# Optimization experiments

Measured on AMD Instinct MI355X. Metric: run time of the kernel, lower is better.

## Reference

```python
import jax, jax.numpy as jnp
import numpy as np

B, N, D, H, L = 2, 2048, 128, 8, 3
V = 32          # NUM_ATOM_TYPES (assumed)
DH = D // H
SCALE = 1.0 / (DH ** 0.5)
NEG = -1e9      # stands in for -inf in the additive attention mask
EPS = 1e-5


def _ln(x, g, b):
    m = x.mean(-1, keepdims=True)
    v = ((x - m) ** 2).mean(-1, keepdims=True)
    return (x - m) / jnp.sqrt(v + EPS) * g + b


def setup_inputs() -> dict:
    key = jax.random.key(0)
    ks = jax.random.split(key, 24)
    nrm = lambda k, shape, std=0.02: jax.random.normal(k, shape, jnp.float32) * std
    atom_embed = nrm(ks[0], (V, D)).at[0].set(0.0)  # padding_idx = 0
    cons_embed = nrm(ks[1], (1, 1, D))
    in_w = nrm(ks[2], (D, D)); in_b = jnp.zeros((D,), jnp.float32)
    qkv_w = nrm(ks[3], (L, 3 * D, D)); qkv_b = jnp.zeros((L, 3 * D), jnp.float32)
    out_w = nrm(ks[4], (L, D, D)); out_b = jnp.zeros((L, D), jnp.float32)
    ln1_g = jnp.ones((L, D), jnp.float32); ln1_b = jnp.zeros((L, D), jnp.float32)
    ln2_g = jnp.ones((L, D), jnp.float32); ln2_b = jnp.zeros((L, D), jnp.float32)
    ff1_w = nrm(ks[5], (L, 4 * D, D)); ff1_b = jnp.zeros((L, 4 * D), jnp.float32)
    ff2_w = nrm(ks[6], (L, D, 4 * D)); ff2_b = jnp.zeros((L, D), jnp.float32)
    struct_bias = nrm(ks[7], (L,), 0.5)  # scalar per layer (init 0 in torch; randomized to exercise the path)
    head_ln_g = jnp.ones((D,), jnp.float32); head_ln_b = jnp.zeros((D,), jnp.float32)
    head_w = nrm(ks[8], (1, D)); head_b = jnp.zeros((1,), jnp.float32)
    is_atom = jax.random.bernoulli(ks[9], 0.5, (B, N))
    atom_id = jax.random.randint(ks[10], (B, N), 0, V)
    mask = jax.random.bernoulli(ks[11], 0.9, (B, N))
    adjacency = (jax.random.uniform(ks[12], (B, N, N)) < 0.002).astype(jnp.float32)
    adjacency = jnp.maximum(adjacency, jnp.eye(N, dtype=jnp.float32)[None])  # self-loops
    root_idx = jax.random.randint(ks[13], (B,), 0, N)
    return dict(atom_embed=atom_embed, cons_embed=cons_embed, in_w=in_w, in_b=in_b,
                qkv_w=qkv_w, qkv_b=qkv_b, out_w=out_w, out_b=out_b,
                ln1_g=ln1_g, ln1_b=ln1_b, ln2_g=ln2_g, ln2_b=ln2_b,
                ff1_w=ff1_w, ff1_b=ff1_b, ff2_w=ff2_w, ff2_b=ff2_b,
                struct_bias=struct_bias, head_ln_g=head_ln_g, head_ln_b=head_ln_b,
                head_w=head_w, head_b=head_b, adjacency=adjacency,
                is_atom=is_atom, atom_id=atom_id, mask=mask, root_idx=root_idx)


def reference(atom_embed, cons_embed, in_w, in_b, qkv_w, qkv_b, out_w, out_b,
              ln1_g, ln1_b, ln2_g, ln2_b, ff1_w, ff1_b, ff2_w, ff2_b,
              struct_bias, head_ln_g, head_ln_b, head_w, head_b,
              adjacency, is_atom, atom_id, mask, root_idx):
    # node embeddings
    ae = atom_embed[jnp.clip(atom_id, 0, V - 1)]                     # [B,N,D]
    h = jnp.where(is_atom[..., None], ae, jnp.broadcast_to(cons_embed, (B, N, D)))
    h = h @ in_w.T + in_b
    # additive attention mask: valid pairs OK; invalid query rows attend only to self
    pair_ok = mask[:, :, None] & mask[:, None, :]
    eye = jnp.eye(N, dtype=bool)[None]
    ok = pair_ok | ((~mask)[:, :, None] & eye)
    am = jnp.where(ok, 0.0, NEG).astype(jnp.float32)                 # [B,N,N]
    for i in range(L):
        x = _ln(h, ln1_g[i], ln1_b[i])
        qkv = (x @ qkv_w[i].T + qkv_b[i]).reshape(B, N, 3, H, DH)
        q, k, v = (jnp.transpose(qkv[:, :, j], (0, 2, 1, 3)) for j in range(3))  # [B,H,N,DH]
        scores = jnp.einsum('bhqd,bhkd->bhqk', q, k) * SCALE \
                 + struct_bias[i] * adjacency[:, None] + am[:, None]
        attn = jax.nn.softmax(scores, axis=-1)
        o = jnp.einsum('bhqk,bhkd->bhqd', attn, v)
        o = jnp.transpose(o, (0, 2, 1, 3)).reshape(B, N, D)
        h = h + (o @ out_w[i].T + out_b[i])
        x2 = _ln(h, ln2_g[i], ln2_b[i])
        f = jax.nn.gelu(x2 @ ff1_w[i].T + ff1_b[i], approximate=False)
        h = h + (f @ ff2_w[i].T + ff2_b[i])
    pooled = h[jnp.arange(B), root_idx]                              # [B,D]
    p = _ln(pooled, head_ln_g, head_ln_b)
    return (p @ head_w.T + head_b)[:, 0]                             # [B]
```

## Files before the change

### kernel.cpp

```cpp
#include <hip/hip_runtime.h>
#include <cmath>

#define NB 2
#define NN 2048
#define ND 128
#define NH 8
#define NL 3
#define NV 32
#define NDH 16
#define LN_EPS 1e-5f
#define QSCALE 0.36067376022224085f

typedef __bf16 bf8_t __attribute__((ext_vector_type(8)));
typedef __bf16 bf4_t __attribute__((ext_vector_type(4)));
typedef float f4x __attribute__((ext_vector_type(4)));
typedef float f16x __attribute__((ext_vector_type(16)));

struct CastArgs {
  const float* s[5];
  __bf16* d[5];
  int startblk[5];
};
__global__ __launch_bounds__(256) void prep_kernel(
    CastArgs a, const float* __restrict__ adj, unsigned long long* __restrict__ abits,
    const int* __restrict__ mask, unsigned long long* __restrict__ mbits) {
  int blk = blockIdx.x;
  int lane = threadIdx.x & 63;
  if (blk < 592) {
    int seg = 0;
#pragma unroll
    for (int i = 1; i < 5; i++) seg += (blk >= a.startblk[i]) ? 1 : 0;
    int i4 = (blk - a.startblk[seg]) * 256 + threadIdx.x;
    float4 v = ((const float4*)a.s[seg])[i4];
    bf4_t p = {(__bf16)v.x, (__bf16)v.y, (__bf16)v.z, (__bf16)v.w};
    ((bf4_t*)a.d[seg])[i4] = p;
  } else if (blk < 592 + 8192) {
    int g = ((blk - 592) * 4 + (threadIdx.x >> 6)) * 4;
    const float* p = adj + (size_t)g * 64 + lane;
    unsigned long long w0 = __ballot(p[0] != 0.0f);
    unsigned long long w1 = __ballot(p[64] != 0.0f);
    unsigned long long w2 = __ballot(p[128] != 0.0f);
    unsigned long long w3 = __ballot(p[192] != 0.0f);
    if (lane == 0) {
      abits[g] = w0; abits[g + 1] = w1; abits[g + 2] = w2; abits[g + 3] = w3;
    }
  } else {
    int g = (blk - 8784) * 4 + (threadIdx.x >> 6);
    int v = mask[g * 64 + lane];
    unsigned long long bal = __ballot(v != 0);
    if (lane == 0) mbits[g] = bal;
  }
}

__global__ __launch_bounds__(512) void fused0_kernel(
    const float* __restrict__ atom_embed, const float* __restrict__ cons_embed,
    const int* __restrict__ is_atom, const int* __restrict__ atom_id,
    const __bf16* __restrict__ W1, const float* __restrict__ b1,
    float* __restrict__ Hout,
    const float* __restrict__ lng, const float* __restrict__ lnb,
    const __bf16* __restrict__ W2, const float* __restrict__ b2,
    __bf16* __restrict__ Qb, __bf16* __restrict__ Kb, __bf16* __restrict__ Vt) {
  __shared__ __bf16 Xs[16][136];
  __shared__ float Hs[16][132];
  __shared__ __bf16 X2[16][136];
  int m0 = blockIdx.x * 16;
  int t = threadIdx.x;
  int lane = t & 63, w = t >> 6;
  int l15 = lane & 15, quad = lane >> 4;
  int wrow = w * 16 + l15;

  {
    int r = t >> 5, c = t & 31;
    int row = m0 + r;
    int id = atom_id[row];
    id = id < 0 ? 0 : (id > NV - 1 ? NV - 1 : id);
    const float* src = is_atom[row] ? (atom_embed + (size_t)id * ND) : cons_embed;
    float4 v = *(const float4*)&src[c * 4];
    bf4_t p = {(__bf16)v.x, (__bf16)v.y, (__bf16)v.z, (__bf16)v.w};
    *(bf4_t*)&Xs[r][c * 4] = p;
  }

  bf8_t wcur[4], wnxt[4];
  auto issue = [&](int i, bf8_t* dst) {
    const __bf16* base = (i == 0) ? W1 : (W2 + (size_t)(i - 1) * 128 * 128);
    const __bf16* p = base + (size_t)wrow * 128 + quad * 8;
#pragma unroll
    for (int kk = 0; kk < 4; kk++) dst[kk] = *(const bf8_t*)(p + kk * 32);
  };
  issue(0, wcur);
  __syncthreads();

  for (int i = 0; i < 4; i++) {
    if (i + 1 < 4) issue(i + 1, wnxt);
    if (i == 0) {
      f4x a1 = {0.f, 0.f, 0.f, 0.f};
#pragma unroll
      for (int kk = 0; kk < 4; kk++) {
        bf8_t a = *(const bf8_t*)&Xs[l15][kk * 32 + quad * 8];
        a1 = __builtin_amdgcn_mfma_f32_16x16x32_bf16(a, wcur[kk], a1, 0, 0, 0);
      }
      int n = wrow;
      float bv = b1[n];
#pragma unroll
      for (int r = 0; r < 4; r++) {
        int m = quad * 4 + r;
        float v = a1[r] + bv;
        Hout[(size_t)(m0 + m) * ND + n] = v;
        Hs[m][n] = v;
      }
      __syncthreads();
      {
        int r = t >> 5, c = t & 31;
        float4 v = *(const float4*)&Hs[r][c * 4];
        float s1 = v.x + v.y + v.z + v.w;
        float s2 = v.x * v.x + v.y * v.y + v.z * v.z + v.w * v.w;
#pragma unroll
        for (int m = 16; m >= 1; m >>= 1) {
          s1 += __shfl_xor(s1, m, 64);
          s2 += __shfl_xor(s2, m, 64);
        }
        float mean = s1 * (1.0f / ND);
        float var = s2 * (1.0f / ND) - mean * mean;
        float rstd = rsqrtf(var + LN_EPS);
        float4 gg = *(const float4*)&lng[c * 4];
        float4 bb = *(const float4*)&lnb[c * 4];
        bf4_t p;
        p[0] = (__bf16)((v.x - mean) * rstd * gg.x + bb.x);
        p[1] = (__bf16)((v.y - mean) * rstd * gg.y + bb.y);
        p[2] = (__bf16)((v.z - mean) * rstd * gg.z + bb.z);
        p[3] = (__bf16)((v.w - mean) * rstd * gg.w + bb.w);
        *(bf4_t*)&X2[r][c * 4] = p;
      }
      __syncthreads();
    } else {
      int nc = i - 1;
      f4x a2 = {0.f, 0.f, 0.f, 0.f};
#pragma unroll
      for (int kk = 0; kk < 4; kk++) {
        bf8_t a = *(const bf8_t*)&X2[l15][kk * 32 + quad * 8];
        a2 = __builtin_amdgcn_mfma_f32_16x16x32_bf16(a, wcur[kk], a2, 0, 0, 0);
      }
      int n = nc * 128 + wrow;
      float bv = b2[n];
#pragma unroll
      for (int r = 0; r < 4; r++) {
        int m = m0 + quad * 4 + r;
        float v = a2[r] + bv;
        if (n < ND) Qb[(size_t)m * ND + n] = (__bf16)(v * QSCALE);
        else if (n < 2 * ND) Kb[(size_t)m * ND + n - ND] = (__bf16)v;
        else {
          int c2 = n - 2 * ND, hh = c2 >> 4, d0 = c2 & 15;
          int bb2 = m >> 11, nn = m & 2047;
          Vt[((size_t)((bb2 * NH + hh) * NDH + d0)) * NN + nn] = (__bf16)v;
        }
      }
    }
#pragma unroll
    for (int kk = 0; kk < 4; kk++) wcur[kk] = wnxt[kk];
  }
}

template <int LAST>
__global__ __launch_bounds__(512) void layer_kernel(
    const __bf16* __restrict__ Ob,
    const __bf16* __restrict__ Wout, const float* __restrict__ bout,
    const float* __restrict__ Hin, float* __restrict__ Hout,
    const float* __restrict__ ln2g, const float* __restrict__ ln2b,
    const __bf16* __restrict__ Wff1, const float* __restrict__ bff1,
    const __bf16* __restrict__ Wff2, const float* __restrict__ bff2,
    const float* __restrict__ ln1g, const float* __restrict__ ln1b,
    const __bf16* __restrict__ Wqkv, const float* __restrict__ bqkv,
    __bf16* __restrict__ Qb, __bf16* __restrict__ Kb, __bf16* __restrict__ Vt,
    const int* __restrict__ root_idx, const float* __restrict__ hg,
    const float* __restrict__ hbt, const float* __restrict__ hwp,
    const float* __restrict__ hbp, float* __restrict__ outp) {
  __shared__ __bf16 Xs[16][136];
  __shared__ float Hs[16][132];
  __shared__ __bf16 X2[16][136];
  __shared__ __bf16 Fs[16][520];
  int m0 = blockIdx.x * 16;
  int t = threadIdx.x;
  int lane = t & 63, w = t >> 6;
  int l15 = lane & 15, quad = lane >> 4;
  int wrow = w * 16 + l15;
  const int T = LAST ? 9 : 12;

  {
    int r = t >> 5, c = t & 31;
    *(bf4_t*)&Xs[r][c * 4] = *(const bf4_t*)&Ob[(size_t)(m0 + r) * ND + c * 4];
  }

  bf8_t wcur[4], wnxt[4];
  auto issue = [&](int i, bf8_t* dst) {
    const __bf16* p;
    if (i == 0)     p = Wout + (size_t)wrow * 128 + quad * 8;
    else if (i < 5) p = Wff1 + ((size_t)((i - 1) * 128 + wrow)) * 128 + quad * 8;
    else if (i < 9) p = Wff2 + (size_t)wrow * 512 + (i - 5) * 128 + quad * 8;
    else            p = Wqkv + ((size_t)((i - 9) * 128 + wrow)) * 128 + quad * 8;
#pragma unroll
    for (int kk = 0; kk < 4; kk++) dst[kk] = *(const bf8_t*)(p + kk * 32);
  };
  issue(0, wcur);
  __syncthreads();

  auto do_ln = [&](const float* g_, const float* b_) {
    int r = t >> 5, c = t & 31;
    float4 v = *(const float4*)&Hs[r][c * 4];
    float s1 = v.x + v.y + v.z + v.w;
    float s2 = v.x * v.x + v.y * v.y + v.z * v.z + v.w * v.w;
#pragma unroll
    for (int m = 16; m >= 1; m >>= 1) {
      s1 += __shfl_xor(s1, m, 64);
      s2 += __shfl_xor(s2, m, 64);
    }
    float mean = s1 * (1.0f / ND);
    float var = s2 * (1.0f / ND) - mean * mean;
    float rstd = rsqrtf(var + LN_EPS);
    float4 gg = *(const float4*)&g_[c * 4];
    float4 bb = *(const float4*)&b_[c * 4];
    bf4_t p;
    p[0] = (__bf16)((v.x - mean) * rstd * gg.x + bb.x);
    p[1] = (__bf16)((v.y - mean) * rstd * gg.y + bb.y);
    p[2] = (__bf16)((v.z - mean) * rstd * gg.z + bb.z);
    p[3] = (__bf16)((v.w - mean) * rstd * gg.w + bb.w);
    *(bf4_t*)&X2[r][c * 4] = p;
  };

  f4x acc2 = {0.f, 0.f, 0.f, 0.f};
  for (int i = 0; i < T; i++) {
    if (i + 1 < T) issue(i + 1, wnxt);
    if (i == 0) {
      f4x a1 = {0.f, 0.f, 0.f, 0.f};
#pragma unroll
      for (int kk = 0; kk < 4; kk++) {
        bf8_t a = *(const bf8_t*)&Xs[l15][kk * 32 + quad * 8];
        a1 = __builtin_amdgcn_mfma_f32_16x16x32_bf16(a, wcur[kk], a1, 0, 0, 0);
      }
      int n = wrow;
      float bv = bout[n];
#pragma unroll
      for (int r = 0; r < 4; r++) {
        int m = quad * 4 + r;
        Hs[m][n] = a1[r] + bv + Hin[(size_t)(m0 + m) * ND + n];
      }
      __syncthreads();
      do_ln(ln2g, ln2b);
      __syncthreads();
    } else if (i < 5) {
      int c = i - 1;
      f4x a1 = {0.f, 0.f, 0.f, 0.f};
#pragma unroll
      for (int kk = 0; kk < 4; kk++) {
        bf8_t a = *(const bf8_t*)&X2[l15][kk * 32 + quad * 8];
        a1 = __builtin_amdgcn_mfma_f32_16x16x32_bf16(a, wcur[kk], a1, 0, 0, 0);
      }
      int n = wrow;
      float bv = bff1[c * 128 + n];
#pragma unroll
      for (int r = 0; r < 4; r++) {
        float v = a1[r] + bv;
        v = 0.5f * v * (1.0f + erff(v * 0.70710678118f));
        Fs[quad * 4 + r][c * 128 + n] = (__bf16)v;
      }
      if (i == 4) __syncthreads();
    } else if (i < 9) {
      int j = i - 5;
#pragma unroll
      for (int kk = 0; kk < 4; kk++) {
        bf8_t a = *(const bf8_t*)&Fs[l15][j * 128 + kk * 32 + quad * 8];
        acc2 = __builtin_amdgcn_mfma_f32_16x16x32_bf16(a, wcur[kk], acc2, 0, 0, 0);
      }
      if (j == 3) {
        int n = wrow;
        float bv = bff2[n];
#pragma unroll
        for (int r = 0; r < 4; r++) {
          int m = quad * 4 + r;
          float v = acc2[r] + bv + Hs[m][n];
          Hs[m][n] = v;
          Hout[(size_t)(m0 + m) * ND + n] = v;
        }
        __syncthreads();
        if constexpr (!LAST) {
          do_ln(ln1g, ln1b);
          __syncthreads();
        }
      }
    } else {
      int nc = i - 9;
      f4x a2 = {0.f, 0.f, 0.f, 0.f};
#pragma unroll
      for (int kk = 0; kk < 4; kk++) {
        bf8_t a = *(const bf8_t*)&X2[l15][kk * 32 + quad * 8];
        a2 = __builtin_amdgcn_mfma_f32_16x16x32_bf16(a, wcur[kk], a2, 0, 0, 0);
      }
      int n = nc * 128 + wrow;
      float bv = bqkv[n];
#pragma unroll
      for (int r = 0; r < 4; r++) {
        int m = m0 + quad * 4 + r;
        float v = a2[r] + bv;
        if (n < ND) Qb[(size_t)m * ND + n] = (__bf16)(v * QSCALE);
        else if (n < 2 * ND) Kb[(size_t)m * ND + n - ND] = (__bf16)v;
        else {
          int c2 = n - 2 * ND, hh = c2 >> 4, d0 = c2 & 15;
          int bb2 = m >> 11, nn = m & 2047;
          Vt[((size_t)((bb2 * NH + hh) * NDH + d0)) * NN + nn] = (__bf16)v;
        }
      }
    }
#pragma unroll
    for (int kk = 0; kk < 4; kk++) wcur[kk] = wnxt[kk];
  }

  if constexpr (LAST) {
    if (w < NB) {
      int rt = root_idx[w];
      int rglob = w * NN + rt;
      if (rglob >= m0 && rglob < m0 + 16) {
        int r = rglob - m0;
        float v0 = Hs[r][2 * lane], v1 = Hs[r][2 * lane + 1];
        float s1 = v0 + v1, s2 = v0 * v0 + v1 * v1;
#pragma unroll
        for (int m = 32; m >= 1; m >>= 1) {
          s1 += __shfl_xor(s1, m, 64);
          s2 += __shfl_xor(s2, m, 64);
        }
        float mean = s1 * (1.0f / ND);
        float var = s2 * (1.0f / ND) - mean * mean;
        float rstd = rsqrtf(var + LN_EPS);
        float p0 = (v0 - mean) * rstd * hg[2 * lane] + hbt[2 * lane];
        float p1 = (v1 - mean) * rstd * hg[2 * lane + 1] + hbt[2 * lane + 1];
        float part = p0 * hwp[2 * lane] + p1 * hwp[2 * lane + 1];
#pragma unroll
        for (int m = 32; m >= 1; m >>= 1) part += __shfl_xor(part, m, 64);
        if (lane == 0) outp[w] = part + hbp[0];
      }
    }
  }
}

__global__ __launch_bounds__(512) void attn_kernel(
    const __bf16* __restrict__ Qb, const __bf16* __restrict__ Kb,
    const __bf16* __restrict__ Vt, const unsigned int* __restrict__ adjbits,
    const unsigned int* __restrict__ maskbits, const int* __restrict__ mask,
    const float* __restrict__ sbias, int layer, __bf16* __restrict__ o) {
  int b = blockIdx.z, hh = blockIdx.y, q0 = blockIdx.x * 32;
  int wave = threadIdx.x >> 6;
  int lane = threadIdx.x & 63;
  int l31 = lane & 31, hi = lane >> 5;
  int l15 = lane & 15, quad = lane >> 4;
  float esb = __expf(sbias[layer]);
  const int bN = b * NN;
  const int kw0 = wave * 256;

  __shared__ __bf16 Pbuf[8][32][40];
  __shared__ float Ored[8][32][17];
  __shared__ float Lred[8][32];

  bf8_t Qf = *(const bf8_t*)(Qb + (size_t)(bN + q0 + l31) * ND + hh * NDH + hi * 8);

  int q = q0 + l31;
  int mq = mask[bN + q];
  const unsigned int* adjp = adjbits + (size_t)(bN + q) * (NN / 32) + (kw0 >> 5);
  const unsigned int* mbp = maskbits + (bN + kw0) / 32;
  const __bf16* kp = Kb + (size_t)(bN + kw0 + l31) * ND + hh * NDH + hi * 8;
  const __bf16* vp = Vt + (size_t)((b * NH + hh) * NDH + l15) * NN + kw0 + quad * 8;

  int dq = q - kw0;
  int tsel = dq >> 5;
  unsigned int selfw = 1u << (dq & 31);
  int sh4 = hi * 4;

  f4x Olo = {0.f, 0.f, 0.f, 0.f}, Ohi = {0.f, 0.f, 0.f, 0.f};
  float ls = 0.f;

  bf8_t Kf = *(const bf8_t*)kp;
  bf8_t Vf = *(const bf8_t*)vp;
  unsigned int aw = adjp[0];
  unsigned int mkw = mbp[0];

  for (int t = 0; t < 8; t++) {
    bf8_t Kn = Kf, Vn = Vf;
    unsigned int awn = aw, mkn = mkw;
    if (t < 7) {
      kp += 32 * ND;
      Kn = *(const bf8_t*)kp;
      Vn = *(const bf8_t*)(vp + (t + 1) * 32);
      awn = adjp[t + 1];
      mkn = mbp[t + 1];
    }
    f16x S = {0.f, 0.f, 0.f, 0.f, 0.f, 0.f, 0.f, 0.f,
              0.f, 0.f, 0.f, 0.f, 0.f, 0.f, 0.f, 0.f};
    S = __builtin_amdgcn_mfma_f32_32x32x16_bf16(Kf, Qf, S, 0, 0, 0);
    unsigned int okw = mq ? mkw : ((t == tsel) ? selfw : 0u);
    unsigned int wa = (aw & okw) >> sh4;
    unsigned int okh = okw >> sh4;
#pragma unroll
    for (int gg = 0; gg < 4; gg++) {
      bf4_t pk;
#pragma unroll
      for (int r = 0; r < 4; r++) {
        int c = gg * 8 + r;
        float e = __builtin_amdgcn_exp2f(S[gg * 4 + r]);
        float wgt = ((wa >> c) & 1) ? esb : (((okh >> c) & 1) ? 1.0f : 0.0f);
        float p = e * wgt;
        ls += p;
        pk[r] = (__bf16)p;
      }
      *(bf4_t*)&Pbuf[wave][l31][sh4 + gg * 8] = pk;
    }
    asm volatile("s_waitcnt lgkmcnt(0)" ::: "memory");
    bf8_t Plo = *(const bf8_t*)&Pbuf[wave][l15][quad * 8];
    bf8_t Phi = *(const bf8_t*)&Pbuf[wave][16 + l15][quad * 8];
    Olo = __builtin_amdgcn_mfma_f32_16x16x32_bf16(Plo, Vf, Olo, 0, 0, 0);
    Ohi = __builtin_amdgcn_mfma_f32_16x16x32_bf16(Phi, Vf, Ohi, 0, 0, 0);
    Kf = Kn; Vf = Vn; aw = awn; mkw = mkn;
  }

  ls += __shfl_xor(ls, 32, 64);
  if (hi == 0) Lred[wave][l31] = ls;
#pragma unroll
  for (int r = 0; r < 4; r++) {
    Ored[wave][quad * 4 + r][l15] = Olo[r];
    Ored[wave][16 + quad * 4 + r][l15] = Ohi[r];
  }
  __syncthreads();
  int row = threadIdx.x >> 4, col = threadIdx.x & 15;
  float s = 0.f, L = 0.f;
#pragma unroll
  for (int p = 0; p < 8; p++) {
    s += Ored[p][row][col];
    L += Lred[p][row];
  }
  o[(size_t)(bN + q0 + row) * ND + hh * NDH + col] = (__bf16)(s / L);
}

extern "C" void kernel_launch(void* const* d_in, const int* in_sizes, int n_in,
                              void* d_out, int out_size, void* d_ws, size_t ws_size,
                              hipStream_t stream) {
  const float* atom_embed = (const float*)d_in[0];
  const float* cons_embed = (const float*)d_in[1];
  const float* in_w  = (const float*)d_in[2];
  const float* in_b  = (const float*)d_in[3];
  const float* qkv_w = (const float*)d_in[4];
  const float* qkv_b = (const float*)d_in[5];
  const float* out_w = (const float*)d_in[6];
  const float* out_b = (const float*)d_in[7];
  const float* ln1_g = (const float*)d_in[8];
  const float* ln1_b = (const float*)d_in[9];
  const float* ln2_g = (const float*)d_in[10];
  const float* ln2_b = (const float*)d_in[11];
  const float* ff1_w = (const float*)d_in[12];
  const float* ff1_b = (const float*)d_in[13];
  const float* ff2_w = (const float*)d_in[14];
  const float* ff2_b = (const float*)d_in[15];
  const float* sbias = (const float*)d_in[16];
  const float* hg    = (const float*)d_in[17];
  const float* hbt   = (const float*)d_in[18];
  const float* hw    = (const float*)d_in[19];
  const float* hb    = (const float*)d_in[20];
  const float* adj   = (const float*)d_in[21];
  const int* is_atom = (const int*)d_in[22];
  const int* atom_id = (const int*)d_in[23];
  const int* mask    = (const int*)d_in[24];
  const int* root_idx= (const int*)d_in[25];
  float* out = (float*)d_out;

  const int MR = NB * NN;
  float* hA = (float*)d_ws;
  float* hB = hA + MR * ND;
  __bf16* Qb   = (__bf16*)(hB + MR * ND);
  __bf16* Kb   = Qb + MR * ND;
  __bf16* Vt   = Kb + MR * ND;
  __bf16* wbin = Vt + MR * ND;
  __bf16* wbqkv= wbin + ND * ND;
  __bf16* wbout= wbqkv + NL * 384 * ND;
  __bf16* wbff1= wbout + NL * ND * ND;
  __bf16* wbff2= wbff1 + NL * 512 * ND;
  unsigned int* adjb = (unsigned int*)(wbff2 + NL * ND * 512);
  unsigned int* mskb = adjb + NB * NN * NN / 32;
  __bf16* ob = (__bf16*)(mskb + 128);

  CastArgs ca;
  ca.s[0] = in_w;  ca.d[0] = wbin;  ca.startblk[0] = 0;
  ca.s[1] = qkv_w; ca.d[1] = wbqkv; ca.startblk[1] = 16;
  ca.s[2] = out_w; ca.d[2] = wbout; ca.startblk[2] = 160;
  ca.s[3] = ff1_w; ca.d[3] = wbff1; ca.startblk[3] = 208;
  ca.s[4] = ff2_w; ca.d[4] = wbff2; ca.startblk[4] = 400;
  prep_kernel<<<8800, 256, 0, stream>>>(ca, adj, (unsigned long long*)adjb,
                                        mask, (unsigned long long*)mskb);

  fused0_kernel<<<dim3(MR / 16), 512, 0, stream>>>(
      atom_embed, cons_embed, is_atom, atom_id,
      wbin, in_b, hA, ln1_g, ln1_b, wbqkv, qkv_b, Qb, Kb, Vt);

  const float* hin[3]  = {hA, hB, hA};
  float* hout[3]       = {hB, hA, hB};
  for (int i = 0; i < NL; i++) {
    attn_kernel<<<dim3(NN / 32, NH, NB), 512, 0, stream>>>(
        Qb, Kb, Vt, adjb, mskb, mask, sbias, i, ob);
    if (i < NL - 1) {
      layer_kernel<0><<<dim3(MR / 16), 512, 0, stream>>>(
          ob, wbout + (size_t)i * ND * ND, out_b + i * ND, hin[i], hout[i],
          ln2_g + i * ND, ln2_b + i * ND,
          wbff1 + (size_t)i * 512 * ND, ff1_b + i * 512,
          wbff2 + (size_t)i * ND * 512, ff2_b + i * ND,
          ln1_g + (i + 1) * ND, ln1_b + (i + 1) * ND,
          wbqkv + (size_t)(i + 1) * 384 * ND, qkv_b + (i + 1) * 384,
          Qb, Kb, Vt,
          nullptr, nullptr, nullptr, nullptr, nullptr, nullptr);
    } else {
      layer_kernel<1><<<dim3(MR / 16), 512, 0, stream>>>(
          ob, wbout + (size_t)i * ND * ND, out_b + i * ND, hin[i], hout[i],
          ln2_g + i * ND, ln2_b + i * ND,
          wbff1 + (size_t)i * 512 * ND, ff1_b + i * 512,
          wbff2 + (size_t)i * ND * 512, ff2_b + i * ND,
          nullptr, nullptr, nullptr, nullptr,
          nullptr, nullptr, nullptr,
          root_idx, hg, hbt, hw, hb, out);
    }
  }
}
```

Measured before the change: 259.6 us.

## Fold key mask into an extra MFMA and patch adjacency entries sparsely

Instead of computing a per-element weight (struct-bias exponent, mask, or zero) for every score, a second MFMA adds a large negative offset to masked keys, so exp2 yields zero for them. Invalid-query self entries are then written directly, and the rare adjacency bits are handled in a sparse loop that rescales the affected P entries in LDS. This removes per-element select logic from the exp loop but adds an extra MFMA per tile, a data-dependent loop, and extra LDS read-modify-write traffic. The large-offset masking relies on the chosen bf16 constants driving exp2 to zero.

```diff
diff --git a/kernel.cpp b/kernel.cpp
--- a/kernel.cpp
+++ b/kernel.cpp
@@ -351,6 +351,7 @@
   int l31 = lane & 31, hi = lane >> 5;
   int l15 = lane & 15, quad = lane >> 4;
   float esb = __expf(sbias[layer]);
+  float esbm1 = esb - 1.0f;
   const int bN = b * NN;
   const int kw0 = wave * 256;
 
@@ -369,8 +370,14 @@
 
   int dq = q - kw0;
   int tsel = dq >> 5;
-  unsigned int selfw = 1u << (dq & 31);
   int sh4 = hi * 4;
+
+  union { bf8_t v; unsigned int u[4]; } Qmu;
+  {
+    unsigned int qw0 = (mq ? 0x4300u : 0u) | (0xC300u << 16);
+    Qmu.u[0] = hi ? 0u : qw0;
+    Qmu.u[1] = 0u; Qmu.u[2] = 0u; Qmu.u[3] = 0u;
+  }
 
   f4x Olo = {0.f, 0.f, 0.f, 0.f}, Ohi = {0.f, 0.f, 0.f, 0.f};
   float ls = 0.f;
@@ -390,25 +397,40 @@
       awn = adjp[t + 1];
       mkn = mbp[t + 1];
     }
+    union { bf8_t v; unsigned int u[4]; } Mfu;
+    {
+      unsigned int mw0 = (((mkw >> l31) & 1u) ? 0x3F80u : 0u) | (0x3F80u << 16);
+      Mfu.u[0] = hi ? 0u : mw0;
+      Mfu.u[1] = 0u; Mfu.u[2] = 0u; Mfu.u[3] = 0u;
+    }
     f16x S = {0.f, 0.f, 0.f, 0.f, 0.f, 0.f, 0.f, 0.f,
               0.f, 0.f, 0.f, 0.f, 0.f, 0.f, 0.f, 0.f};
     S = __builtin_amdgcn_mfma_f32_32x32x16_bf16(Kf, Qf, S, 0, 0, 0);
-    unsigned int okw = mq ? mkw : ((t == tsel) ? selfw : 0u);
-    unsigned int wa = (aw & okw) >> sh4;
-    unsigned int okh = okw >> sh4;
+    S = __builtin_amdgcn_mfma_f32_32x32x16_bf16(Mfu.v, Qmu.v, S, 0, 0, 0);
 #pragma unroll
     for (int gg = 0; gg < 4; gg++) {
       bf4_t pk;
 #pragma unroll
       for (int r = 0; r < 4; r++) {
-        int c = gg * 8 + r;
         float e = __builtin_amdgcn_exp2f(S[gg * 4 + r]);
-        float wgt = ((wa >> c) & 1) ? esb : (((okh >> c) & 1) ? 1.0f : 0.0f);
-        float p = e * wgt;
-        ls += p;
-        pk[r] = (__bf16)p;
+        ls += e;
+        pk[r] = (__bf16)e;
       }
       *(bf4_t*)&Pbuf[wave][l31][sh4 + gg * 8] = pk;
+    }
+    asm volatile("s_waitcnt lgkmcnt(0)" ::: "memory");
+    if (!mq && t == tsel && hi == 0) {
+      Pbuf[wave][l31][dq & 31] = (__bf16)1.0f;
+      ls += 1.0f;
+    }
+    unsigned int fb = ((aw & mkw) >> sh4) & 0x0f0f0f0fu;
+    while (fb) {
+      int c = __builtin_ctz(fb);
+      fb &= fb - 1;
+      __bf16* ap = &Pbuf[wave][l31][sh4 + c];
+      float old = (float)*ap;
+      *ap = (__bf16)(old * esb);
+      ls += old * esbm1;
     }
     asm volatile("s_waitcnt lgkmcnt(0)" ::: "memory");
     bf8_t Plo = *(const bf8_t*)&Pbuf[wave][l15][quad * 8];
```

Measured after the change: 258.7 us. Within noise of the previous version (-0.3%).
